# Kernel optimization log

Measured on AMD Instinct MI355X. Metric: run time of the kernel, lower is better.

## Reference

```python
import jax, jax.numpy as jnp
import numpy as np

TOP_K = 2


def setup_inputs() -> dict:
    key = jax.random.key(0)
    k1, k2, k3, k4, k5 = jax.random.split(key, 5)
    B, S, H, I, E = 2, 2048, 1024, 1408, 8
    scale = 0.02
    return {
        "hidden_states": jax.random.normal(k1, (B, S, H), dtype=jnp.float32),
        "router_w": jax.random.normal(k2, (E, H), dtype=jnp.float32) * scale,
        "w_gate": jax.random.normal(k3, (E, I, H), dtype=jnp.float32) * scale,
        "w_up": jax.random.normal(k4, (E, I, H), dtype=jnp.float32) * scale,
        "w_down": jax.random.normal(k5, (E, H, I), dtype=jnp.float32) * scale,
    }


def reference(hidden_states, router_w, w_gate, w_up, w_down):
    B, S, H = hidden_states.shape
    E = router_w.shape[0]
    x = hidden_states.reshape(-1, H)  # [T, H]

    # Router: softmax over experts, take top-k, renormalize.
    probs = jax.nn.softmax(x @ router_w.T, axis=-1)          # [T, E]
    topk_w, topk_idx = jax.lax.top_k(probs, TOP_K)            # [T, k]
    topk_w = topk_w / (jnp.sum(topk_w, axis=-1, keepdims=True) + 1e-20)

    # Dense combine weights: zero for non-selected experts -> identical math
    # to the masked gather/scatter loop in the original module.
    combine = jnp.sum(
        topk_w[..., None] * jax.nn.one_hot(topk_idx, E, dtype=topk_w.dtype),
        axis=1,
    )  # [T, E]

    out = jnp.zeros_like(x)
    for e in range(E):  # small fixed expert count; unrolled under jit
        g = x @ w_gate[e].T                                   # [T, I]
        u = x @ w_up[e].T                                     # [T, I]
        ye = (jax.nn.silu(g) * u) @ w_down[e].T               # [T, H]
        out = out + combine[:, e:e + 1] * ye
    return out.reshape(B, S, H)
```

## Files before the change

### kernel.cpp

```cpp
#include <hip/hip_runtime.h>
#include <hip/hip_bf16.h>

#define T_TOK 4096
#define H_DIM 1024
#define I_DIM 1408
#define E_NUM 8
#define P_CAP 8192

typedef __bf16 bf16;
typedef __bf16 bf16x4 __attribute__((ext_vector_type(4)));
typedef __bf16 bf16x8 __attribute__((ext_vector_type(8)));
typedef float  f32x4  __attribute__((ext_vector_type(4)));

__device__ __forceinline__ void load_lds16(const void* g, void* l) {
  __builtin_amdgcn_global_load_lds((const __attribute__((address_space(1))) void*)g,
                                   (__attribute__((address_space(3))) void*)l, 16, 0, 0);
}

__global__ __launch_bounds__(256) void cast_f2b(const float* __restrict__ s,
                                                bf16* __restrict__ d, int n) {
  int i = (blockIdx.x * 256 + threadIdx.x) * 4;
  if (i >= n) return;
  float4 v = *(const float4*)(s + i);
  bf16x4 o;
  o.x = (bf16)v.x; o.y = (bf16)v.y; o.z = (bf16)v.z; o.w = (bf16)v.w;
  *(bf16x4*)(d + i) = o;
}

__global__ __launch_bounds__(256) void router_kernel(const float* __restrict__ x,
                                                     const float* __restrict__ rw,
                                                     int* __restrict__ tidx,
                                                     float* __restrict__ tw) {
  int t = blockIdx.x * 4 + (threadIdx.x >> 6);
  int lane = threadIdx.x & 63;
  const float* xr = x + (size_t)t * H_DIM;
  float acc[E_NUM];
#pragma unroll
  for (int e = 0; e < E_NUM; ++e) acc[e] = 0.f;
  for (int c = lane; c < H_DIM; c += 64) {
    float xv = xr[c];
#pragma unroll
    for (int e = 0; e < E_NUM; ++e) acc[e] += xv * rw[e * H_DIM + c];
  }
#pragma unroll
  for (int e = 0; e < E_NUM; ++e)
    for (int s = 32; s > 0; s >>= 1) acc[e] += __shfl_down(acc[e], s, 64);
  if (lane == 0) {
    int a = 0;
#pragma unroll
    for (int e = 1; e < E_NUM; ++e) if (acc[e] > acc[a]) a = e;
    int b = (a == 0) ? 1 : 0;
#pragma unroll
    for (int e = 0; e < E_NUM; ++e) if (e != a && acc[e] > acc[b]) b = e;
    float pb = expf(acc[b] - acc[a]);
    float inv = 1.f / (1.f + pb);
    tidx[t * 2] = a; tidx[t * 2 + 1] = b;
    tw[t * 2] = inv; tw[t * 2 + 1] = pb * inv;
  }
}

__global__ __launch_bounds__(256) void bucket_kernel(const int* __restrict__ tidx,
                                                     const float* __restrict__ tw,
                                                     int* __restrict__ pair_tok,
                                                     float* __restrict__ pair_w,
                                                     int* __restrict__ counts,
                                                     int* __restrict__ offsets) {
  __shared__ int sc[E_NUM], so[E_NUM], scur[E_NUM];
  int tid = threadIdx.x;
  if (tid < E_NUM) sc[tid] = 0;
  __syncthreads();
  for (int p = tid; p < T_TOK * 2; p += 256) atomicAdd(&sc[tidx[p]], 1);
  __syncthreads();
  if (tid == 0) {
    int run = 0;
    for (int e = 0; e < E_NUM; ++e) { so[e] = run; run += sc[e]; }
  }
  __syncthreads();
  if (tid < E_NUM) scur[tid] = so[tid];
  __syncthreads();
  for (int t = tid; t < T_TOK; t += 256) {
#pragma unroll
    for (int k = 0; k < 2; ++k) {
      int e = tidx[t * 2 + k];
      int pos = atomicAdd(&scur[e], 1);
      pair_tok[pos] = t;
      pair_w[pos] = tw[t * 2 + k];
    }
  }
  if (tid < E_NUM) { counts[tid] = sc[tid]; offsets[tid] = so[tid]; }
}

__global__ __launch_bounds__(256, 2)
void gemm1_kernel(const bf16* __restrict__ xb, const bf16* __restrict__ wgb,
                  const bf16* __restrict__ wub, const int* __restrict__ pair_tok,
                  const int* __restrict__ counts, const int* __restrict__ offsets,
                  bf16* __restrict__ mid) {
  const int e = blockIdx.z;
  const int cnt = counts[e];
  const int m0 = blockIdx.y << 7;
  if (m0 >= cnt) return;
  const int off = offsets[e];
  const int n0 = blockIdx.x << 7;

  __shared__ bf16 As[128 * 64];
  __shared__ bf16 Bgs[128 * 64];
  __shared__ bf16 Bus[128 * 64];

  const int tid = threadIdx.x;
  const int wave = tid >> 6;
  const int lane = tid & 63;
  const int wm = (wave >> 1) << 6;
  const int wn = (wave & 1) << 6;

  const bf16* wg_e = wgb + (size_t)e * (I_DIM * H_DIM);
  const bf16* wu_e = wub + (size_t)e * (I_DIM * H_DIM);

  int arow[4], acs[4], atok[4];
#pragma unroll
  for (int j = 0; j < 4; ++j) {
    int seg = ((wave << 2) + j) * 64 + lane;
    arow[j] = seg >> 3;
    acs[j]  = (seg & 7) << 3;
    int gr = m0 + arow[j];
    int cr = gr < cnt ? gr : cnt - 1;
    atok[j] = pair_tok[off + cr];
  }

  f32x4 accg[4][4], accu[4][4];
#pragma unroll
  for (int i = 0; i < 4; ++i)
#pragma unroll
    for (int j = 0; j < 4; ++j) {
      accg[i][j] = (f32x4){0.f, 0.f, 0.f, 0.f};
      accu[i][j] = (f32x4){0.f, 0.f, 0.f, 0.f};
    }

  for (int k0 = 0; k0 < H_DIM; k0 += 64) {
#pragma unroll
    for (int j = 0; j < 4; ++j) {
      int base = ((wave << 2) + j) << 9;
      load_lds16(xb + (size_t)atok[j] * H_DIM + k0 + acs[j], As + base);
      load_lds16(wg_e + (size_t)(n0 + arow[j]) * H_DIM + k0 + acs[j], Bgs + base);
      load_lds16(wu_e + (size_t)(n0 + arow[j]) * H_DIM + k0 + acs[j], Bus + base);
    }
    __syncthreads();
#pragma unroll
    for (int ks = 0; ks < 2; ++ks) {
      const int kc = (ks << 5) + ((lane >> 4) << 3);
      const int lr = lane & 15;
      bf16x8 a[4], bg[4], bu[4];
#pragma unroll
      for (int i = 0; i < 4; ++i)
        a[i] = *(const bf16x8*)(As + (wm + (i << 4) + lr) * 64 + kc);
#pragma unroll
      for (int j = 0; j < 4; ++j) {
        bg[j] = *(const bf16x8*)(Bgs + (wn + (j << 4) + lr) * 64 + kc);
        bu[j] = *(const bf16x8*)(Bus + (wn + (j << 4) + lr) * 64 + kc);
      }
#pragma unroll
      for (int i = 0; i < 4; ++i)
#pragma unroll
        for (int j = 0; j < 4; ++j) {
          accg[i][j] = __builtin_amdgcn_mfma_f32_16x16x32_bf16(a[i], bg[j], accg[i][j], 0, 0, 0);
          accu[i][j] = __builtin_amdgcn_mfma_f32_16x16x32_bf16(a[i], bu[j], accu[i][j], 0, 0, 0);
        }
    }
    __syncthreads();
  }

  const int lr = lane & 15, qd = lane >> 4;
#pragma unroll
  for (int i = 0; i < 4; ++i) {
#pragma unroll
    for (int r = 0; r < 4; ++r) {
      int row = wm + (i << 4) + (qd << 2) + r;
      int gr = m0 + row;
      if (gr < cnt) {
        bf16* mrow = mid + (size_t)(off + gr) * I_DIM + n0 + wn;
#pragma unroll
        for (int j = 0; j < 4; ++j) {
          float g = accg[i][j][r], u = accu[i][j][r];
          float s = g / (1.f + __expf(-g));
          mrow[(j << 4) + lr] = (bf16)(s * u);
        }
      }
    }
  }
}

__global__ __launch_bounds__(256, 2)
void gemm2_kernel(const bf16* __restrict__ mid, const bf16* __restrict__ wdb,
                  const int* __restrict__ pair_tok, const float* __restrict__ pair_w,
                  const int* __restrict__ counts, const int* __restrict__ offsets,
                  float* __restrict__ out) {
  const int e = blockIdx.z;
  const int cnt = counts[e];
  const int m0 = blockIdx.y << 7;
  if (m0 >= cnt) return;
  const int off = offsets[e];
  const int n0 = blockIdx.x << 7;

  __shared__ bf16 As[128 * 64];
  __shared__ bf16 Bs[128 * 64];

  const int tid = threadIdx.x;
  const int wave = tid >> 6;
  const int lane = tid & 63;
  const int wm = (wave >> 1) << 6;
  const int wn = (wave & 1) << 6;

  const bf16* wd_e = wdb + (size_t)e * (H_DIM * I_DIM);

  int arow[4], acs[4];
  size_t apos[4];
#pragma unroll
  for (int j = 0; j < 4; ++j) {
    int seg = ((wave << 2) + j) * 64 + lane;
    arow[j] = seg >> 3;
    acs[j]  = (seg & 7) << 3;
    int gr = m0 + arow[j];
    int cr = gr < cnt ? gr : cnt - 1;
    apos[j] = (size_t)(off + cr) * I_DIM + acs[j];
  }

  f32x4 acc[4][4];
#pragma unroll
  for (int i = 0; i < 4; ++i)
#pragma unroll
    for (int j = 0; j < 4; ++j) acc[i][j] = (f32x4){0.f, 0.f, 0.f, 0.f};

  for (int k0 = 0; k0 < I_DIM; k0 += 64) {
#pragma unroll
    for (int j = 0; j < 4; ++j) {
      int base = ((wave << 2) + j) << 9;
      load_lds16(mid + apos[j] + k0, As + base);
      load_lds16(wd_e + (size_t)(n0 + arow[j]) * I_DIM + k0 + acs[j], Bs + base);
    }
    __syncthreads();
#pragma unroll
    for (int ks = 0; ks < 2; ++ks) {
      const int kc = (ks << 5) + ((lane >> 4) << 3);
      const int lr = lane & 15;
      bf16x8 a[4], b[4];
#pragma unroll
      for (int i = 0; i < 4; ++i)
        a[i] = *(const bf16x8*)(As + (wm + (i << 4) + lr) * 64 + kc);
#pragma unroll
      for (int j = 0; j < 4; ++j)
        b[j] = *(const bf16x8*)(Bs + (wn + (j << 4) + lr) * 64 + kc);
#pragma unroll
      for (int i = 0; i < 4; ++i)
#pragma unroll
        for (int j = 0; j < 4; ++j)
          acc[i][j] = __builtin_amdgcn_mfma_f32_16x16x32_bf16(a[i], b[j], acc[i][j], 0, 0, 0);
    }
    __syncthreads();
  }

  const int lr = lane & 15, qd = lane >> 4;
#pragma unroll
  for (int i = 0; i < 4; ++i) {
#pragma unroll
    for (int r = 0; r < 4; ++r) {
      int row = wm + (i << 4) + (qd << 2) + r;
      int gr = m0 + row;
      if (gr < cnt) {
        int t = pair_tok[off + gr];
        float w = pair_w[off + gr];
        float* orow = out + (size_t)t * H_DIM + n0 + wn;
#pragma unroll
        for (int j = 0; j < 4; ++j)
          atomicAdd(orow + (j << 4) + lr, w * acc[i][j][r]);
      }
    }
  }
}

extern "C" void kernel_launch(void* const* d_in, const int* in_sizes, int n_in,
                              void* d_out, int out_size, void* d_ws, size_t ws_size,
                              hipStream_t stream) {
  const float* x  = (const float*)d_in[0];
  const float* rw = (const float*)d_in[1];
  const float* wg = (const float*)d_in[2];
  const float* wu = (const float*)d_in[3];
  const float* wd = (const float*)d_in[4];
  float* out = (float*)d_out;

  char* ws = (char*)d_ws;
  bf16*  xb      = (bf16*)(ws);
  bf16*  wgb     = (bf16*)(ws + 8388608);
  bf16*  wub     = (bf16*)(ws + 31457280);
  bf16*  wdb     = (bf16*)(ws + 54525952);
  bf16*  mid     = (bf16*)(ws + 77594624);
  int*   tidx    = (int*)(ws + 100663296);
  float* tw      = (float*)(ws + 100696064);
  int*   ptok    = (int*)(ws + 100728832);
  float* pw      = (float*)(ws + 100761600);
  int*   counts  = (int*)(ws + 100794368);
  int*   offsets = (int*)(ws + 100794400);

  hipMemsetAsync(d_out, 0, (size_t)T_TOK * H_DIM * sizeof(float), stream);
  cast_f2b<<<4096, 256, 0, stream>>>(x, xb, T_TOK * H_DIM);
  cast_f2b<<<11264, 256, 0, stream>>>(wg, wgb, E_NUM * I_DIM * H_DIM);
  cast_f2b<<<11264, 256, 0, stream>>>(wu, wub, E_NUM * I_DIM * H_DIM);
  cast_f2b<<<11264, 256, 0, stream>>>(wd, wdb, E_NUM * H_DIM * I_DIM);
  router_kernel<<<1024, 256, 0, stream>>>(x, rw, tidx, tw);
  bucket_kernel<<<1, 256, 0, stream>>>(tidx, tw, ptok, pw, counts, offsets);
  gemm1_kernel<<<dim3(11, 32, 8), 256, 0, stream>>>(xb, wgb, wub, ptok, counts, offsets, mid);
  gemm2_kernel<<<dim3(8, 32, 8), 256, 0, stream>>>(mid, wdb, ptok, pw, counts, offsets, out);
}
```

Baseline: 361.6 us.

## Swizzle LDS tiles, compact expert block grid, and fuse cast kernels

```diff
diff --git a/kernel.cpp b/kernel.cpp
--- a/kernel.cpp
+++ b/kernel.cpp
@@ -6,6 +6,7 @@
 #define I_DIM 1408
 #define E_NUM 8
 #define P_CAP 8192
+#define GRID_Y 71
 
 typedef __bf16 bf16;
 typedef __bf16 bf16x4 __attribute__((ext_vector_type(4)));
@@ -17,10 +18,19 @@
                                    (__attribute__((address_space(3))) void*)l, 16, 0, 0);
 }
 
-__global__ __launch_bounds__(256) void cast_f2b(const float* __restrict__ s,
-                                                bf16* __restrict__ d, int n) {
-  int i = (blockIdx.x * 256 + threadIdx.x) * 4;
-  if (i >= n) return;
+__global__ __launch_bounds__(256) void cast_all(const float* __restrict__ x,
+                                                const float* __restrict__ wg,
+                                                const float* __restrict__ wu,
+                                                const float* __restrict__ wd,
+                                                bf16* __restrict__ xb, bf16* __restrict__ wgb,
+                                                bf16* __restrict__ wub, bf16* __restrict__ wdb) {
+  int b = blockIdx.x;
+  const float* s; bf16* d; int base;
+  if (b < 4096)       { s = x;  d = xb;  base = b; }
+  else if (b < 15360) { s = wg; d = wgb; base = b - 4096; }
+  else if (b < 26624) { s = wu; d = wub; base = b - 15360; }
+  else                { s = wd; d = wdb; base = b - 26624; }
+  size_t i = ((size_t)base * 256 + threadIdx.x) * 4;
   float4 v = *(const float4*)(s + i);
   bf16x4 o;
   o.x = (bf16)v.x; o.y = (bf16)v.y; o.z = (bf16)v.z; o.w = (bf16)v.w;
@@ -64,7 +74,9 @@
                                                      int* __restrict__ pair_tok,
                                                      float* __restrict__ pair_w,
                                                      int* __restrict__ counts,
-                                                     int* __restrict__ offsets) {
+                                                     int* __restrict__ offsets,
+                                                     int* __restrict__ blk2e,
+                                                     int* __restrict__ blk2m) {
   __shared__ int sc[E_NUM], so[E_NUM], scur[E_NUM];
   int tid = threadIdx.x;
   if (tid < E_NUM) sc[tid] = 0;
@@ -72,8 +84,12 @@
   for (int p = tid; p < T_TOK * 2; p += 256) atomicAdd(&sc[tidx[p]], 1);
   __syncthreads();
   if (tid == 0) {
-    int run = 0;
-    for (int e = 0; e < E_NUM; ++e) { so[e] = run; run += sc[e]; }
+    int run = 0, nb = 0;
+    for (int e = 0; e < E_NUM; ++e) {
+      so[e] = run; run += sc[e];
+      for (int m = 0; m * 128 < sc[e]; ++m) { blk2e[nb] = e; blk2m[nb] = m; ++nb; }
+    }
+    for (; nb < GRID_Y; ++nb) { blk2e[nb] = -1; blk2m[nb] = 0; }
   }
   __syncthreads();
   if (tid < E_NUM) scur[tid] = so[tid];
@@ -94,11 +110,12 @@
 void gemm1_kernel(const bf16* __restrict__ xb, const bf16* __restrict__ wgb,
                   const bf16* __restrict__ wub, const int* __restrict__ pair_tok,
                   const int* __restrict__ counts, const int* __restrict__ offsets,
+                  const int* __restrict__ blk2e, const int* __restrict__ blk2m,
                   bf16* __restrict__ mid) {
-  const int e = blockIdx.z;
+  const int e = blk2e[blockIdx.y];
+  if (e < 0) return;
   const int cnt = counts[e];
-  const int m0 = blockIdx.y << 7;
-  if (m0 >= cnt) return;
+  const int m0 = blk2m[blockIdx.y] << 7;
   const int off = offsets[e];
   const int n0 = blockIdx.x << 7;
 
@@ -119,9 +136,10 @@
 #pragma unroll
   for (int j = 0; j < 4; ++j) {
     int seg = ((wave << 2) + j) * 64 + lane;
-    arow[j] = seg >> 3;
-    acs[j]  = (seg & 7) << 3;
-    int gr = m0 + arow[j];
+    int row = seg >> 3;
+    arow[j] = row;
+    acs[j]  = ((seg & 7) ^ (row & 7)) << 3;
+    int gr = m0 + row;
     int cr = gr < cnt ? gr : cnt - 1;
     atok[j] = pair_tok[off + cr];
   }
@@ -134,6 +152,10 @@
       accg[i][j] = (f32x4){0.f, 0.f, 0.f, 0.f};
       accu[i][j] = (f32x4){0.f, 0.f, 0.f, 0.f};
     }
+
+  const int lr = lane & 15;
+  const int sw = lr & 7;
+  const int qd = lane >> 4;
 
   for (int k0 = 0; k0 < H_DIM; k0 += 64) {
 #pragma unroll
@@ -146,8 +168,7 @@
     __syncthreads();
 #pragma unroll
     for (int ks = 0; ks < 2; ++ks) {
-      const int kc = (ks << 5) + ((lane >> 4) << 3);
-      const int lr = lane & 15;
+      const int kc = (((ks << 2) + qd) ^ sw) << 3;
       bf16x8 a[4], bg[4], bu[4];
 #pragma unroll
       for (int i = 0; i < 4; ++i)
@@ -168,7 +189,6 @@
     __syncthreads();
   }
 
-  const int lr = lane & 15, qd = lane >> 4;
 #pragma unroll
   for (int i = 0; i < 4; ++i) {
 #pragma unroll
@@ -192,11 +212,12 @@
 void gemm2_kernel(const bf16* __restrict__ mid, const bf16* __restrict__ wdb,
                   const int* __restrict__ pair_tok, const float* __restrict__ pair_w,
                   const int* __restrict__ counts, const int* __restrict__ offsets,
+                  const int* __restrict__ blk2e, const int* __restrict__ blk2m,
                   float* __restrict__ out) {
-  const int e = blockIdx.z;
+  const int e = blk2e[blockIdx.y];
+  if (e < 0) return;
   const int cnt = counts[e];
-  const int m0 = blockIdx.y << 7;
-  if (m0 >= cnt) return;
+  const int m0 = blk2m[blockIdx.y] << 7;
   const int off = offsets[e];
   const int n0 = blockIdx.x << 7;
 
@@ -216,9 +237,10 @@
 #pragma unroll
   for (int j = 0; j < 4; ++j) {
     int seg = ((wave << 2) + j) * 64 + lane;
-    arow[j] = seg >> 3;
-    acs[j]  = (seg & 7) << 3;
-    int gr = m0 + arow[j];
+    int row = seg >> 3;
+    arow[j] = row;
+    acs[j]  = ((seg & 7) ^ (row & 7)) << 3;
+    int gr = m0 + row;
     int cr = gr < cnt ? gr : cnt - 1;
     apos[j] = (size_t)(off + cr) * I_DIM + acs[j];
   }
@@ -228,6 +250,10 @@
   for (int i = 0; i < 4; ++i)
 #pragma unroll
     for (int j = 0; j < 4; ++j) acc[i][j] = (f32x4){0.f, 0.f, 0.f, 0.f};
+
+  const int lr = lane & 15;
+  const int sw = lr & 7;
+  const int qd = lane >> 4;
 
   for (int k0 = 0; k0 < I_DIM; k0 += 64) {
 #pragma unroll
@@ -239,8 +265,7 @@
     __syncthreads();
 #pragma unroll
     for (int ks = 0; ks < 2; ++ks) {
-      const int kc = (ks << 5) + ((lane >> 4) << 3);
-      const int lr = lane & 15;
+      const int kc = (((ks << 2) + qd) ^ sw) << 3;
       bf16x8 a[4], b[4];
 #pragma unroll
       for (int i = 0; i < 4; ++i)
@@ -257,7 +282,6 @@
     __syncthreads();
   }
 
-  const int lr = lane & 15, qd = lane >> 4;
 #pragma unroll
   for (int i = 0; i < 4; ++i) {
 #pragma unroll
@@ -298,14 +322,13 @@
   float* pw      = (float*)(ws + 100761600);
   int*   counts  = (int*)(ws + 100794368);
   int*   offsets = (int*)(ws + 100794400);
+  int*   blk2e   = (int*)(ws + 100794432);
+  int*   blk2m   = (int*)(ws + 100794752);
 
   hipMemsetAsync(d_out, 0, (size_t)T_TOK * H_DIM * sizeof(float), stream);
-  cast_f2b<<<4096, 256, 0, stream>>>(x, xb, T_TOK * H_DIM);
-  cast_f2b<<<11264, 256, 0, stream>>>(wg, wgb, E_NUM * I_DIM * H_DIM);
-  cast_f2b<<<11264, 256, 0, stream>>>(wu, wub, E_NUM * I_DIM * H_DIM);
-  cast_f2b<<<11264, 256, 0, stream>>>(wd, wdb, E_NUM * H_DIM * I_DIM);
+  cast_all<<<37888, 256, 0, stream>>>(x, wg, wu, wd, xb, wgb, wub, wdb);
   router_kernel<<<1024, 256, 0, stream>>>(x, rw, tidx, tw);
-  bucket_kernel<<<1, 256, 0, stream>>>(tidx, tw, ptok, pw, counts, offsets);
-  gemm1_kernel<<<dim3(11, 32, 8), 256, 0, stream>>>(xb, wgb, wub, ptok, counts, offsets, mid);
-  gemm2_kernel<<<dim3(8, 32, 8), 256, 0, stream>>>(mid, wdb, ptok, pw, counts, offsets, out);
-}
+  bucket_kernel<<<1, 256, 0, stream>>>(tidx, tw, ptok, pw, counts, offsets, blk2e, blk2m);
+  gemm1_kernel<<<dim3(11, GRID_Y), 256, 0, stream>>>(xb, wgb, wub, ptok, counts, offsets, blk2e, blk2m, mid);
+  gemm2_kernel<<<dim3(8, GRID_Y), 256, 0, stream>>>(mid, wdb, ptok, pw, counts, offsets, blk2e, blk2m, out);
+}
```

Measured after the change: 345.8 us. 4.4% less time.
